# Performance work log

Measured on AMD Instinct MI355X. Metric: run time of the kernel, lower is better.

Reference implementation:

```python
import jax, jax.numpy as jnp
import numpy as np

K_NN = 9  # kernel_size: neighbors per node (includes self, dist 0)


def knn_edges(feat):
    """feat: (B, C, N). Replicates DenseDilatedKnnGraph (dilation=1):
    L2-normalize over channels, dense pairwise sq-distance, top-k nearest."""
    nrm = jnp.sqrt(jnp.sum(feat * feat, axis=1, keepdims=True))
    xn = feat / jnp.maximum(nrm, 1e-12)            # F.normalize(dim=1)
    xt = jnp.swapaxes(xn, 1, 2)                    # (B, N, C)
    sq = jnp.sum(xt * xt, axis=-1)                 # (B, N)
    dist = sq[:, :, None] + sq[:, None, :] - 2.0 * jnp.einsum('bnc,bmc->bnm', xt, xt)
    _, nn_idx = jax.lax.top_k(-dist, K_NN)         # (B, N, k)
    center = jnp.broadcast_to(jnp.arange(nn_idx.shape[1], dtype=nn_idx.dtype)[None, :, None], nn_idx.shape)
    return nn_idx, center                          # (x_j sources, x_i targets)


def reference(x, W0, W1, bias):
    B, C, H, W = x.shape
    N = H * W
    NB = B * N
    feat = x.reshape(B, C, N)
    # KNN graph is built on detached features in the torch source
    x_j, x_i = knn_edges(jax.lax.stop_gradient(feat))
    E = B * N * K_NN
    # faithful to source: torch.linspace(0, B, steps=E, dtype=int64) batch offsets
    count = jnp.linspace(0.0, float(B), E).astype(jnp.int32)
    src = x_j.reshape(-1).astype(jnp.int32) + count * N
    dst = x_i.reshape(-1).astype(jnp.int32) + count * N
    valid = (src < NB) & (dst < NB)                # drop the out-of-range tail edge
    # flat_nodes: (B, C, H, W) -> (B*H*W, C), node id = b*HW + pixel
    nodes = jnp.swapaxes(feat, 1, 2).reshape(NB, C)
    # ChebConv K=2, sym norm, lambda_max=2: Tx0 = x, Tx1 = -(D^-1/2 A D^-1/2) x
    w = valid.astype(nodes.dtype)
    deg = jax.ops.segment_sum(w, src, num_segments=NB)
    dinv = jnp.where(deg > 0, jax.lax.rsqrt(jnp.maximum(deg, 1.0)), 0.0)
    norm = -(dinv[src] * w * dinv[dst])            # scaled-Laplacian edge weights
    msg = norm[:, None] * nodes[src]               # (E, C) gather + weight
    Tx1 = jax.ops.segment_sum(msg, dst, num_segments=NB)
    return nodes @ W0 + Tx1 @ W1 + bias


def setup_inputs() -> dict:
    key = jax.random.key(0)
    k1, k2, k3, k4 = jax.random.split(key, 4)
    B, C, H, W = 8, 48, 64, 64
    Cout = 48
    s = 1.0 / np.sqrt(C)
    return {
        'x': jax.random.normal(k1, (B, C, H, W), dtype=jnp.float32),
        'W0': jax.random.normal(k2, (C, Cout), dtype=jnp.float32) * s,
        'W1': jax.random.normal(k3, (C, Cout), dtype=jnp.float32) * s,
        'bias': jax.random.normal(k4, (Cout,), dtype=jnp.float32) * 0.01,
    }
```

## Files before the change

kernel.cpp:

```cpp
#include <hip/hip_runtime.h>

#define BATCH 8
#define CH    48
#define NPTS  4096
#define NBN   (BATCH*NPTS)
#define KNN   9
#define NCAND 12

typedef unsigned short u16;
typedef unsigned int   u32;
typedef unsigned long long u64;
typedef __bf16 bf16x8 __attribute__((ext_vector_type(8)));
typedef float  f32x4  __attribute__((ext_vector_type(4)));

__device__ __forceinline__ float bf2f(u16 v) { return __uint_as_float(((u32)v) << 16); }
__device__ __forceinline__ u16 f2bf(float f) {
  u32 u = __float_as_uint(f);
  u = (u + 0x7fffu + ((u >> 16) & 1u)) >> 16;
  return (u16)u;
}

__global__ __launch_bounds__(256)
void k_prep(const float* __restrict__ x, float* __restrict__ xraw,
            float* __restrict__ xn, float* __restrict__ csq,
            u16* __restrict__ Abuf, u16* __restrict__ Bbuf,
            int* __restrict__ deg) {
  int node = blockIdx.x * 256 + threadIdx.x;
  deg[node] = 0;
  int b = node >> 12, n = node & (NPTS - 1);
  const float* xb = x + (size_t)b * CH * NPTS;
  float f[CH];
#pragma unroll
  for (int c = 0; c < CH; ++c) f[c] = xb[(size_t)c * NPTS + n];
  float a0 = 0, a1 = 0, a2 = 0, a3 = 0;
#pragma unroll
  for (int k = 0; k < CH; k += 4) {
    a0 += f[k] * f[k]; a1 += f[k+1] * f[k+1];
    a2 += f[k+2] * f[k+2]; a3 += f[k+3] * f[k+3];
  }
  float nrm = fmaxf(sqrtf((a0 + a1) + (a2 + a3)), 1e-12f);
  float xv[CH];
#pragma unroll
  for (int c = 0; c < CH; ++c) xv[c] = f[c] / nrm;
  a0 = a1 = a2 = a3 = 0;
#pragma unroll
  for (int k = 0; k < CH; k += 4) {
    a0 += xv[k] * xv[k]; a1 += xv[k+1] * xv[k+1];
    a2 += xv[k+2] * xv[k+2]; a3 += xv[k+3] * xv[k+3];
  }
  float csqv = (a0 + a1) + (a2 + a3);
  csq[node] = csqv;
  float4* ro = (float4*)(xraw + (size_t)node * CH);
  float4* no = (float4*)(xn   + (size_t)node * CH);
#pragma unroll
  for (int i = 0; i < CH / 4; ++i) {
    ro[i] = make_float4(f[4*i], f[4*i+1], f[4*i+2], f[4*i+3]);
    no[i] = make_float4(xv[4*i], xv[4*i+1], xv[4*i+2], xv[4*i+3]);
  }
  u16 ah[64], al[64];
#pragma unroll
  for (int k = 0; k < CH; ++k) {
    float av = -2.0f * xv[k];
    u16 h = f2bf(av); ah[k] = h; al[k] = f2bf(av - bf2f(h));
  }
  { u16 h = f2bf(csqv); ah[48] = h; al[48] = f2bf(csqv - bf2f(h)); }
#pragma unroll
  for (int k = 49; k < 64; ++k) { ah[k] = 0; al[k] = 0; }
  u16* Bh = Bbuf + (size_t)node * 128;
#pragma unroll
  for (int k = 0; k < CH; ++k) {
    float bv = xv[k];
    u16 h = f2bf(bv); Bh[k] = h; Bh[64 + k] = f2bf(bv - bf2f(h));
  }
  Bh[48] = 0x3F80; Bh[64 + 48] = 0;
#pragma unroll
  for (int k = 49; k < 64; ++k) { Bh[k] = 0; Bh[64 + k] = 0; }
  u16* Ag = Abuf + (size_t)(node >> 4) * 2048 + (size_t)(node & 15) * 8;
#pragma unroll
  for (int v = 0; v < 4; ++v) {
    const u16* src = (v < 2) ? ah : al;
    int koff = (v & 1) * 32;
#pragma unroll
    for (int q = 0; q < 4; ++q) {
      uint4 pk;
      const u16* s = src + koff + q * 8;
      pk.x = (u32)s[0] | ((u32)s[1] << 16);
      pk.y = (u32)s[2] | ((u32)s[3] << 16);
      pk.z = (u32)s[4] | ((u32)s[5] << 16);
      pk.w = (u32)s[6] | ((u32)s[7] << 16);
      *(uint4*)(Ag + v * 512 + q * 128) = pk;
    }
  }
}

#define MED3(d, a, b, c) \
  asm("v_med3_u32 %0, %1, %2, %3" : "=v"(d) : "v"(a), "v"(b), "v"(c))
#define INSERT12(x) do { \
  MED3(s11, s10, s11, x); MED3(s10, s9, s10, x); MED3(s9, s8, s9, x);  \
  MED3(s8,  s7,  s8,  x); MED3(s7,  s6, s7,  x); MED3(s6, s5, s6, x);  \
  MED3(s5,  s4,  s5,  x); MED3(s4,  s3, s4,  x); MED3(s3, s2, s3, x);  \
  MED3(s2,  s1,  s2,  x); MED3(s1,  s0, s1,  x); s0 = min(s0, x);      \
} while (0)

__global__ __launch_bounds__(256, 6)
void k_knn_m(const u16* __restrict__ Abuf, const u16* __restrict__ Bbuf,
             u64* __restrict__ candu) {
  int tid = threadIdx.x;
  int lane = tid & 63;
  int quad = lane >> 4, m16 = lane & 15;
  int panel = blockIdx.x * 4 + (tid >> 6);
  int row = panel * 16 + m16;
  int b4096 = row & ~(NPTS - 1);
  int quarter = blockIdx.y;
  int ct0 = quarter * 64;

  const __bf16* Bb = (const __bf16*)Bbuf + (size_t)row * 128;
  bf16x8 bh0 = *(const bf16x8*)(Bb + quad * 8);
  bf16x8 bh1 = *(const bf16x8*)(Bb + 32 + quad * 8);
  bf16x8 bl0 = *(const bf16x8*)(Bb + 64 + quad * 8);
  bf16x8 bl1 = *(const bf16x8*)(Bb + 96 + quad * 8);

  const __bf16* Ag = (const __bf16*)Abuf + (size_t)(b4096 >> 4) * 2048
                     + (size_t)lane * 8 + (size_t)ct0 * 2048;

  u32 s0=~0u,s1=~0u,s2=~0u,s3=~0u,s4=~0u,s5=~0u,
      s6=~0u,s7=~0u,s8=~0u,s9=~0u,s10=~0u,s11=~0u;

  bf16x8 a0 = *(const bf16x8*)(Ag);
  bf16x8 a1 = *(const bf16x8*)(Ag + 512);
  bf16x8 a2 = *(const bf16x8*)(Ag + 1024);
  bf16x8 a3 = *(const bf16x8*)(Ag + 1536);

  for (int t = 0; t < 64; ++t) {
    const __bf16* apn = Ag + (size_t)((t < 63) ? (t + 1) : 63) * 2048;
    bf16x8 n0 = *(const bf16x8*)(apn);
    bf16x8 n1 = *(const bf16x8*)(apn + 512);
    bf16x8 n2 = *(const bf16x8*)(apn + 1024);
    bf16x8 n3 = *(const bf16x8*)(apn + 1536);

    f32x4 acc = {2.5f, 2.5f, 2.5f, 2.5f};
    acc = __builtin_amdgcn_mfma_f32_16x16x32_bf16(a0, bh0, acc, 0, 0, 0);
    acc = __builtin_amdgcn_mfma_f32_16x16x32_bf16(a1, bh1, acc, 0, 0, 0);
    acc = __builtin_amdgcn_mfma_f32_16x16x32_bf16(a0, bl0, acc, 0, 0, 0);
    acc = __builtin_amdgcn_mfma_f32_16x16x32_bf16(a1, bl1, acc, 0, 0, 0);
    acc = __builtin_amdgcn_mfma_f32_16x16x32_bf16(a2, bh0, acc, 0, 0, 0);
    acc = __builtin_amdgcn_mfma_f32_16x16x32_bf16(a3, bh1, acc, 0, 0, 0);
    int ct = ct0 + t;
#pragma unroll
    for (int r = 0; r < 4; ++r) {
      u32 u = __float_as_uint(acc[r]);
      u32 x = (u & 0xFFFFFC00u) | (u32)((ct << 2) | r);
      INSERT12(x);
    }
    a0 = n0; a1 = n1; a2 = n2; a3 = n3;
  }

  u64* o = candu + (((size_t)row * 4 + quarter) * 4 + quad) * NCAND;
#define EMIT(j, sv) { u32 col = ((sv & 0x3FFu) >> 2) * 16 + quad * 4 + (sv & 3u); \
                      o[j] = ((u64)sv << 12) | (u64)col; }
  EMIT(0, s0)  EMIT(1, s1)  EMIT(2, s2)  EMIT(3, s3)
  EMIT(4, s4)  EMIT(5, s5)  EMIT(6, s6)  EMIT(7, s7)
  EMIT(8, s8)  EMIT(9, s9)  EMIT(10, s10) EMIT(11, s11)
#undef EMIT
}

#define STEP64(si) { u64 _lo = (x < si) ? x : si; u64 _hi = (x < si) ? si : x; \
                     si = _lo; x = _hi; }
__global__ __launch_bounds__(256, 4)
void k_reduce(const u64* __restrict__ candu, u32* __restrict__ cand12) {
  __shared__ u64 ls[64 * 4 * NCAND];
  int tid = threadIdx.x;
  int lr = tid >> 2, q = tid & 3;
  int row = blockIdx.x * 64 + lr;
  const u64* src = candu + (size_t)row * 192 + q * 48;
  u64 t0=~0ull,t1=~0ull,t2=~0ull,t3=~0ull,t4=~0ull,t5=~0ull,
      t6=~0ull,t7=~0ull,t8=~0ull,t9=~0ull,t10=~0ull,t11=~0ull;
  for (int s = 0; s < 48; ++s) {
    u64 x = src[s];
    STEP64(t0) STEP64(t1) STEP64(t2) STEP64(t3) STEP64(t4) STEP64(t5)
    STEP64(t6) STEP64(t7) STEP64(t8) STEP64(t9) STEP64(t10) STEP64(t11)
  }
  u64* lw = ls + (size_t)(lr * 4 + q) * NCAND;
  lw[0]=t0; lw[1]=t1; lw[2]=t2; lw[3]=t3; lw[4]=t4; lw[5]=t5;
  lw[6]=t6; lw[7]=t7; lw[8]=t8; lw[9]=t9; lw[10]=t10; lw[11]=t11;
  __syncthreads();
  if (q == 0) {
    u64 g0=~0ull,g1=~0ull,g2=~0ull,g3=~0ull,g4=~0ull,g5=~0ull,
        g6=~0ull,g7=~0ull,g8=~0ull,g9=~0ull,g10=~0ull,g11=~0ull;
    const u64* lsrc = ls + (size_t)lr * 48;
    for (int s = 0; s < 48; ++s) {
      u64 x = lsrc[s];
      STEP64(g0) STEP64(g1) STEP64(g2) STEP64(g3) STEP64(g4) STEP64(g5)
      STEP64(g6) STEP64(g7) STEP64(g8) STEP64(g9) STEP64(g10) STEP64(g11)
    }
    u32* o = cand12 + (size_t)row * NCAND;
    o[0]=(u32)(g0&0xFFFu); o[1]=(u32)(g1&0xFFFu); o[2]=(u32)(g2&0xFFFu);
    o[3]=(u32)(g3&0xFFFu); o[4]=(u32)(g4&0xFFFu); o[5]=(u32)(g5&0xFFFu);
    o[6]=(u32)(g6&0xFFFu); o[7]=(u32)(g7&0xFFFu); o[8]=(u32)(g8&0xFFFu);
    o[9]=(u32)(g9&0xFFFu); o[10]=(u32)(g10&0xFFFu); o[11]=(u32)(g11&0xFFFu);
  }
}

#define RR 16
__global__ __launch_bounds__(256, 4)
void k_rescore(const float* __restrict__ xn, const float* __restrict__ csq,
               const u32* __restrict__ cand12,
               u16* __restrict__ nn, int* __restrict__ deg) {
  __shared__ float dS[RR * NCAND];
  __shared__ int   iS[RR * NCAND];
  int tid = threadIdx.x;
  int lr = tid >> 4, q = tid & 15;
  int bi = blockIdx.x;
  int row = (bi & 7) * NPTS + (bi >> 3) * RR + lr;
  int b4096 = row & ~(NPTS - 1);
  const float* xnb = xn + (size_t)b4096 * CH;
  if (q < NCAND) {
    float rf[CH];
    const float4* p = (const float4*)(xn + (size_t)row * CH);
#pragma unroll
    for (int i = 0; i < CH / 4; ++i) {
      float4 v = p[i];
      rf[4*i] = v.x; rf[4*i+1] = v.y; rf[4*i+2] = v.z; rf[4*i+3] = v.w;
    }
    float sqn = csq[row];
    int c = (int)(cand12[(size_t)row * NCAND + q] & (NPTS - 1));
    const float4* cp = (const float4*)(xnb + (size_t)c * CH);
    float a0 = 0, a1 = 0, a2 = 0, a3 = 0;
#pragma unroll
    for (int i = 0; i < CH / 4; ++i) {
      float4 v = cp[i];
      a0 += rf[4*i]   * v.x; a1 += rf[4*i+1] * v.y;
      a2 += rf[4*i+2] * v.z; a3 += rf[4*i+3] * v.w;
    }
    float dist = (sqn + csq[b4096 + c]) - 2.0f * ((a0 + a1) + (a2 + a3));
    dS[lr * NCAND + q] = dist;
    iS[lr * NCAND + q] = c;
  }
  __syncthreads();
  if (q == 0) {
    float gd[KNN]; int gi[KNN];
#pragma unroll
    for (int j = 0; j < KNN; ++j) { gd[j] = 3.4e38f; gi[j] = 0x7fffffff; }
    for (int s = 0; s < NCAND; ++s) {
      float dc = dS[lr * NCAND + s]; int ic = iS[lr * NCAND + s];
      if (dc < gd[KNN - 1] || (dc == gd[KNN - 1] && ic < gi[KNN - 1])) {
        gd[KNN - 1] = dc; gi[KNN - 1] = ic;
#pragma unroll
        for (int k2 = KNN - 1; k2 > 0; --k2) {
          bool sw = (gd[k2] < gd[k2 - 1]) ||
                    (gd[k2] == gd[k2 - 1] && gi[k2] < gi[k2 - 1]);
          if (sw) {
            float td = gd[k2]; gd[k2] = gd[k2 - 1]; gd[k2 - 1] = td;
            int ti = gi[k2]; gi[k2] = gi[k2 - 1]; gi[k2 - 1] = ti;
          }
        }
      }
    }
    u16* o = nn + (size_t)row * KNN;
    int jmax = (row == NBN - 1) ? (KNN - 1) : KNN;
#pragma unroll
    for (int j = 0; j < KNN; ++j) o[j] = (u16)(gi[j] & (NPTS - 1));
    for (int j = 0; j < jmax; ++j)
      atomicAdd(&deg[b4096 + (gi[j] & (NPTS - 1))], 1);
  }
}

#define ONB 64
#define LPAD 52
__global__ __launch_bounds__(256)
void k_out_f(const float* __restrict__ xraw, const u16* __restrict__ nn,
             const int* __restrict__ deg,
             const float* __restrict__ W0, const float* __restrict__ W1,
             const float* __restrict__ bias, float* __restrict__ out) {
  __shared__ float w0[CH * CH], w1[CH * CH], bs[CH];
  __shared__ __align__(16) float fS[ONB * LPAD];
  __shared__ __align__(16) float txS[ONB * LPAD];
  __shared__ float dinvS[ONB];
  int tid = threadIdx.x;
  int bi = blockIdx.x;
  int n0 = (bi & 7) * NPTS + (bi >> 3) * ONB;
  int b12 = n0 & ~(NPTS - 1);
  for (int i = tid; i < CH * CH; i += 256) { w0[i] = W0[i]; w1[i] = W1[i]; }
  if (tid < CH) bs[tid] = bias[tid];
  for (int i = tid; i < ONB * 12; i += 256) {
    int ln = i / 12, f4 = i % 12;
    *(float4*)(fS + ln * LPAD + f4 * 4) =
        *(const float4*)(xraw + (size_t)(n0 + ln) * CH + f4 * 4);
  }
  if (tid < ONB) {
    int dg = deg[n0 + tid];
    dinvS[tid] = (dg > 0) ? (1.0f / sqrtf((float)dg)) : 0.0f;
  }
  __syncthreads();

  int ln = tid >> 2, p = tid & 3;
  int node = n0 + ln;
  float dn = dinvS[ln];
  const u16* nrow = nn + (size_t)node * KNN;
  bool full = (node != NBN - 1);
  float tx[12];
#pragma unroll
  for (int i = 0; i < 12; ++i) tx[i] = 0.f;
#pragma unroll
  for (int j = 0; j < KNN; ++j) {
    if (j < KNN - 1 || full) {
      int s = nrow[j] & (NPTS - 1);
      int dgs = deg[b12 + s];
      float ds = (dgs > 0) ? (1.0f / sqrtf((float)dgs)) : 0.0f;
      float w = -(ds * dn);
      const float4* pr = (const float4*)(xraw + (size_t)(b12 + s) * CH + p * 12);
#pragma unroll
      for (int q3 = 0; q3 < 3; ++q3) {
        float4 v = pr[q3];
        tx[q3*4]   += w * v.x; tx[q3*4+1] += w * v.y;
        tx[q3*4+2] += w * v.z; tx[q3*4+3] += w * v.w;
      }
    }
  }
#pragma unroll
  for (int q3 = 0; q3 < 3; ++q3)
    *(float4*)(txS + ln * LPAD + p * 12 + q3 * 4) =
        make_float4(tx[q3*4], tx[q3*4+1], tx[q3*4+2], tx[q3*4+3]);
  __syncthreads();

  float acc[12];
#pragma unroll
  for (int i = 0; i < 12; ++i) acc[i] = bs[p * 12 + i];
  const float* fr = fS + ln * LPAD;
  const float* tr = txS + ln * LPAD;
#pragma unroll
  for (int c = 0; c < CH; ++c) {
    float fc = fr[c];
    const float* wr = w0 + c * CH + p * 12;
#pragma unroll
    for (int i = 0; i < 12; ++i) acc[i] += fc * wr[i];
  }
#pragma unroll
  for (int c = 0; c < CH; ++c) {
    float tc = tr[c];
    const float* wr = w1 + c * CH + p * 12;
#pragma unroll
    for (int i = 0; i < 12; ++i) acc[i] += tc * wr[i];
  }
  float* op = out + (size_t)node * CH + p * 12;
#pragma unroll
  for (int q3 = 0; q3 < 3; ++q3)
    *(float4*)(op + q3 * 4) =
        make_float4(acc[q3*4], acc[q3*4+1], acc[q3*4+2], acc[q3*4+3]);
}

__global__ __launch_bounds__(256)
void k_zero(int* __restrict__ deg) { deg[blockIdx.x * 256 + threadIdx.x] = 0; }

__global__ __launch_bounds__(256)
void k_hist(const u16* __restrict__ nn, int* __restrict__ deg) {
  int node = blockIdx.x * 256 + threadIdx.x;
  int b12 = node & ~(NPTS - 1);
  int jmax = (node == NBN - 1) ? (KNN - 1) : KNN;
  for (int j = 0; j < jmax; ++j)
    atomicAdd(&deg[b12 + (nn[(size_t)node * KNN + j] & (NPTS - 1))], 1);
}

__global__ __launch_bounds__(256)
void k_dinv(const int* __restrict__ deg, float* __restrict__ dinv) {
  int i = blockIdx.x * 256 + threadIdx.x;
  int dg = deg[i];
  dinv[i] = (dg > 0) ? (1.0f / sqrtf((float)dg)) : 0.0f;
}

#define NQ    4
#define QCOLS (NPTS/NQ)
#define TCOLS 32
#define NTILES (QCOLS/TCOLS)
#define RPB   64

__global__ __launch_bounds__(256)
void k_knn_nb(const float* __restrict__ x, u16* __restrict__ nn) {
  __shared__ __align__(16) float tile[NQ * TCOLS * CH];
  __shared__ float nrmS[NQ * TCOLS];
  __shared__ float csq[NQ * TCOLS];
  int tid = threadIdx.x;
  int r0 = blockIdx.x * RPB;
  int b  = r0 >> 12;
  int q  = tid >> 6;
  int lr = tid & 63;
  int n  = (r0 + lr) & (NPTS - 1);
  const float* xb = x + (size_t)b * CH * NPTS;
  float rf[CH];
#pragma unroll
  for (int c = 0; c < CH; ++c) rf[c] = xb[(size_t)c * NPTS + n];
  float sqn;
  {
    float a0 = 0, a1 = 0, a2 = 0, a3 = 0;
#pragma unroll
    for (int k = 0; k < CH; k += 4) {
      a0 += rf[k] * rf[k]; a1 += rf[k+1] * rf[k+1];
      a2 += rf[k+2] * rf[k+2]; a3 += rf[k+3] * rf[k+3];
    }
    float nrm = fmaxf(sqrtf((a0 + a1) + (a2 + a3)), 1e-12f);
#pragma unroll
    for (int c = 0; c < CH; ++c) rf[c] = rf[c] / nrm;
    a0 = a1 = a2 = a3 = 0;
#pragma unroll
    for (int k = 0; k < CH; k += 4) {
      a0 += rf[k] * rf[k]; a1 += rf[k+1] * rf[k+1];
      a2 += rf[k+2] * rf[k+2]; a3 += rf[k+3] * rf[k+3];
    }
    sqn = (a0 + a1) + (a2 + a3);
  }
  float d[KNN]; int id[KNN];
#pragma unroll
  for (int j = 0; j < KNN; ++j) { d[j] = 3.4e38f; id[j] = 0x7fffffff; }
  for (int t = 0; t < NTILES; ++t) {
    __syncthreads();
#pragma unroll
    for (int qq = 0; qq < NQ; ++qq) {
      int colbase = qq * QCOLS + t * TCOLS;
      float* dst = tile + qq * TCOLS * CH;
#pragma unroll
      for (int it = 0; it < 6; ++it) {
        int i = it * 256 + tid;
        int c = i >> 5, p = i & 31;
        dst[p * CH + c] = xb[(size_t)c * NPTS + colbase + p];
      }
    }
    __syncthreads();
    if (tid < NQ * TCOLS) {
      const float* cp = tile + tid * CH;
      float a0 = 0, a1 = 0, a2 = 0, a3 = 0;
#pragma unroll
      for (int k = 0; k < CH; k += 4) {
        float4 v = *(const float4*)(cp + k);
        a0 += v.x * v.x; a1 += v.y * v.y; a2 += v.z * v.z; a3 += v.w * v.w;
      }
      nrmS[tid] = fmaxf(sqrtf((a0 + a1) + (a2 + a3)), 1e-12f);
    }
    __syncthreads();
    for (int i = tid; i < NQ * TCOLS * CH; i += 256)
      tile[i] = tile[i] / nrmS[i / CH];
    __syncthreads();
    if (tid < NQ * TCOLS) {
      const float* cp = tile + tid * CH;
      float a0 = 0, a1 = 0, a2 = 0, a3 = 0;
#pragma unroll
      for (int k = 0; k < CH; k += 4) {
        float4 v = *(const float4*)(cp + k);
        a0 += v.x * v.x; a1 += v.y * v.y; a2 += v.z * v.z; a3 += v.w * v.w;
      }
      csq[tid] = (a0 + a1) + (a2 + a3);
    }
    __syncthreads();
    int cbase = q * QCOLS + t * TCOLS;
    const float* tq = tile + q * TCOLS * CH;
    for (int cc = 0; cc < TCOLS; ++cc) {
      const float* cp = tq + cc * CH;
      float a0 = 0, a1 = 0, a2 = 0, a3 = 0;
#pragma unroll
      for (int k = 0; k < CH; k += 4) {
        float4 v = *(const float4*)(cp + k);
        a0 += rf[k] * v.x; a1 += rf[k+1] * v.y;
        a2 += rf[k+2] * v.z; a3 += rf[k+3] * v.w;
      }
      float dist = (sqn + csq[q * TCOLS + cc]) - 2.0f * ((a0 + a1) + (a2 + a3));
      if (dist < d[KNN - 1]) {
        d[KNN - 1] = dist; id[KNN - 1] = cbase + cc;
#pragma unroll
        for (int k2 = KNN - 1; k2 > 0; --k2) {
          if (d[k2] < d[k2 - 1]) {
            float td = d[k2]; d[k2] = d[k2 - 1]; d[k2 - 1] = td;
            int ti = id[k2]; id[k2] = id[k2 - 1]; id[k2 - 1] = ti;
          }
        }
      }
    }
  }
  __syncthreads();
  float* md = tile;
  int*   mi = (int*)(tile + 256 * KNN);
#pragma unroll
  for (int j = 0; j < KNN; ++j) { md[tid * KNN + j] = d[j]; mi[tid * KNN + j] = id[j]; }
  __syncthreads();
  if (tid < RPB) {
    float fd[KNN]; int fi[KNN];
#pragma unroll
    for (int j = 0; j < KNN; ++j) { fd[j] = 3.4e38f; fi[j] = 0x7fffffff; }
    for (int qq = 0; qq < NQ; ++qq) {
      int s = qq * RPB + tid;
      for (int j = 0; j < KNN; ++j) {
        float dc = md[s * KNN + j]; int ic = mi[s * KNN + j];
        if (dc < fd[KNN - 1]) {
          fd[KNN - 1] = dc; fi[KNN - 1] = ic;
#pragma unroll
          for (int k2 = KNN - 1; k2 > 0; --k2) {
            if (fd[k2] < fd[k2 - 1]) {
              float td = fd[k2]; fd[k2] = fd[k2 - 1]; fd[k2 - 1] = td;
              int ti = fi[k2]; fi[k2] = fi[k2 - 1]; fi[k2 - 1] = ti;
            }
          }
        }
      }
    }
    u16* o = nn + (size_t)(r0 + tid) * KNN;
#pragma unroll
    for (int j = 0; j < KNN; ++j) o[j] = (u16)(fi[j] & (NPTS - 1));
  }
}

__global__ __launch_bounds__(256)
void k_out_nb(const float* __restrict__ x, const u16* __restrict__ nn,
              const float* __restrict__ dinv,
              const float* __restrict__ W0, const float* __restrict__ W1,
              const float* __restrict__ bias, float* __restrict__ out) {
  __shared__ float w0[CH * CH], w1[CH * CH], bs[CH];
  for (int i = threadIdx.x; i < CH * CH; i += 256) { w0[i] = W0[i]; w1[i] = W1[i]; }
  if (threadIdx.x < CH) bs[threadIdx.x] = bias[threadIdx.x];
  __syncthreads();
  int node = blockIdx.x * 256 + threadIdx.x;
  int b = node >> 12, n = node & (NPTS - 1);
  const float* xb = x + (size_t)b * CH * NPTS;
  float f[CH], acc[CH], tx[CH];
#pragma unroll
  for (int c = 0; c < CH; ++c) f[c] = xb[(size_t)c * NPTS + n];
#pragma unroll
  for (int o = 0; o < CH; ++o) acc[o] = bs[o];
#pragma unroll
  for (int c = 0; c < CH; ++c) {
    float fc = f[c];
    const float* wr = w0 + c * CH;
#pragma unroll
    for (int o = 0; o < CH; ++o) acc[o] += fc * wr[o];
  }
#pragma unroll
  for (int c = 0; c < CH; ++c) tx[c] = 0.f;
  float dn = dinv[node];
  int jmax = (node == NBN - 1) ? (KNN - 1) : KNN;
  for (int j = 0; j < jmax; ++j) {
    int s = nn[(size_t)node * KNN + j] & (NPTS - 1);
    float w = -(dinv[(b << 12) + s] * dn);
#pragma unroll
    for (int c = 0; c < CH; ++c) tx[c] += w * xb[(size_t)c * NPTS + s];
  }
#pragma unroll
  for (int c = 0; c < CH; ++c) {
    float tc = tx[c];
    const float* wr = w1 + c * CH;
#pragma unroll
    for (int o = 0; o < CH; ++o) acc[o] += tc * wr[o];
  }
  float4* op = (float4*)(out + (size_t)node * CH);
#pragma unroll
  for (int i = 0; i < CH / 4; ++i)
    op[i] = make_float4(acc[4*i], acc[4*i+1], acc[4*i+2], acc[4*i+3]);
}

extern "C" void kernel_launch(void* const* d_in, const int* in_sizes, int n_in,
                              void* d_out, int out_size, void* d_ws, size_t ws_size,
                              hipStream_t stream) {
  const float* x    = (const float*)d_in[0];
  const float* W0   = (const float*)d_in[1];
  const float* W1   = (const float*)d_in[2];
  const float* bias = (const float*)d_in[3];
  float* out = (float*)d_out;
  char* w = (char*)d_ws;

  const size_t SZ_XN   = (size_t)NBN * CH * 4;
  const size_t SZ_XRAW = (size_t)NBN * CH * 4;
  const size_t SZ_CSQ  = (size_t)NBN * 4;
  const size_t SZ_NN   = (size_t)NBN * KNN * 2;
  const size_t SZ_DEG  = (size_t)NBN * 4;
  const size_t SZ_AB   = (size_t)NBN * 128 * 2;
  const size_t SZ_CU   = (size_t)NBN * 16 * NCAND * 8;
  const size_t SZ_C12  = (size_t)NBN * NCAND * 4;
  const size_t needF = SZ_XN + SZ_XRAW + SZ_CSQ + SZ_NN + SZ_DEG
                     + 2 * SZ_AB + SZ_CU + SZ_C12;

  if (ws_size >= needF) {
    size_t off = 0;
    float* xn   = (float*)(w + off); off += SZ_XN;
    float* xraw = (float*)(w + off); off += SZ_XRAW;
    float* csq  = (float*)(w + off); off += SZ_CSQ;
    u16*   nn   = (u16*)  (w + off); off += SZ_NN;
    int*   deg  = (int*)  (w + off); off += SZ_DEG;
    u16*   Abuf = (u16*)  (w + off); off += SZ_AB;
    u16*   Bbuf = (u16*)  (w + off); off += SZ_AB;
    u64*   candu= (u64*)  (w + off); off += SZ_CU;
    u32*   cand12=(u32*)  (w + off);
    k_prep    <<<NBN / 256, 256, 0, stream>>>(x, xraw, xn, csq, Abuf, Bbuf, deg);
    k_knn_m   <<<dim3(NBN / 64, 4), 256, 0, stream>>>(Abuf, Bbuf, candu);
    k_reduce  <<<NBN / 64, 256, 0, stream>>>(candu, cand12);
    k_rescore <<<NBN / RR, 256, 0, stream>>>(xn, csq, cand12, nn, deg);
    k_out_f   <<<NBN / ONB, 256, 0, stream>>>(xraw, nn, deg, W0, W1, bias, out);
  } else {
    u16*   nn   = (u16*)w;
    int*   deg  = (int*)(w + SZ_NN);
    float* dinv = (float*)(w + SZ_NN + SZ_DEG);
    k_knn_nb <<<NBN / RPB, 256, 0, stream>>>(x, nn);
    k_zero   <<<NBN / 256, 256, 0, stream>>>(deg);
    k_hist   <<<NBN / 256, 256, 0, stream>>>(nn, deg);
    k_dinv   <<<NBN / 256, 256, 0, stream>>>(deg, dinv);
    k_out_nb <<<NBN / 256, 256, 0, stream>>>(x, nn, dinv, W0, W1, bias, out);
  }
}
```

Baseline: 240.1 us.

## Pack candidates into 32-bit keys and unroll KNN tile loop by two

The KNN scoring kernel now packs the full 12-bit column index into the low bits of each 32-bit distance key, so candidates are stored as u32 instead of u64. The reduce kernel then uses v_med3_u32 insertion on 32-bit keys rather than 64-bit compare-swap chains, halving candidate memory traffic and LDS use. The tile loop is unrolled by two with double-buffered A loads to overlap loads with MFMA and the insertion work, and the occupancy hint drops from 6 to 4 waves. Dropping two more mantissa bits from the distance key coarsens the ordering, which may change tie resolution among near-equal candidates.

```diff
diff --git a/kernel.cpp b/kernel.cpp
--- a/kernel.cpp
+++ b/kernel.cpp
@@ -19,6 +19,15 @@
   u = (u + 0x7fffu + ((u >> 16) & 1u)) >> 16;
   return (u16)u;
 }
+
+#define MED3U(d, a, b, c) \
+  asm("v_med3_u32 %0, %1, %2, %3" : "=v"(d) : "v"(a), "v"(b), "v"(c))
+#define INS12(p0,p1,p2,p3,p4,p5,p6,p7,p8,p9,p10,p11,x) do { \
+  MED3U(p11,p10,p11,x); MED3U(p10,p9,p10,x); MED3U(p9,p8,p9,x);  \
+  MED3U(p8, p7, p8, x); MED3U(p7, p6,p7, x); MED3U(p6,p5,p6,x);  \
+  MED3U(p5, p4, p5, x); MED3U(p4, p3,p4, x); MED3U(p3,p2,p3,x);  \
+  MED3U(p2, p1, p2, x); MED3U(p1, p0,p1, x); p0 = min(p0, x);    \
+} while (0)
 
 __global__ __launch_bounds__(256)
 void k_prep(const float* __restrict__ x, float* __restrict__ xraw,
@@ -93,18 +102,9 @@
   }
 }
 
-#define MED3(d, a, b, c) \
-  asm("v_med3_u32 %0, %1, %2, %3" : "=v"(d) : "v"(a), "v"(b), "v"(c))
-#define INSERT12(x) do { \
-  MED3(s11, s10, s11, x); MED3(s10, s9, s10, x); MED3(s9, s8, s9, x);  \
-  MED3(s8,  s7,  s8,  x); MED3(s7,  s6, s7,  x); MED3(s6, s5, s6, x);  \
-  MED3(s5,  s4,  s5,  x); MED3(s4,  s3, s4,  x); MED3(s3, s2, s3, x);  \
-  MED3(s2,  s1,  s2,  x); MED3(s1,  s0, s1,  x); s0 = min(s0, x);      \
-} while (0)
-
-__global__ __launch_bounds__(256, 6)
+__global__ __launch_bounds__(256, 4)
 void k_knn_m(const u16* __restrict__ Abuf, const u16* __restrict__ Bbuf,
-             u64* __restrict__ candu) {
+             u32* __restrict__ candu) {
   int tid = threadIdx.x;
   int lane = tid & 63;
   int quad = lane >> 4, m16 = lane & 15;
@@ -126,78 +126,82 @@
   u32 s0=~0u,s1=~0u,s2=~0u,s3=~0u,s4=~0u,s5=~0u,
       s6=~0u,s7=~0u,s8=~0u,s9=~0u,s10=~0u,s11=~0u;
 
+#define TILE_BODY(A0,A1,A2,A3,CT) do {                                      \
+    f32x4 acc = {2.5f, 2.5f, 2.5f, 2.5f};                                   \
+    acc = __builtin_amdgcn_mfma_f32_16x16x32_bf16(A0, bh0, acc, 0, 0, 0);   \
+    acc = __builtin_amdgcn_mfma_f32_16x16x32_bf16(A1, bh1, acc, 0, 0, 0);   \
+    acc = __builtin_amdgcn_mfma_f32_16x16x32_bf16(A0, bl0, acc, 0, 0, 0);   \
+    acc = __builtin_amdgcn_mfma_f32_16x16x32_bf16(A1, bl1, acc, 0, 0, 0);   \
+    acc = __builtin_amdgcn_mfma_f32_16x16x32_bf16(A2, bh0, acc, 0, 0, 0);   \
+    acc = __builtin_amdgcn_mfma_f32_16x16x32_bf16(A3, bh1, acc, 0, 0, 0);   \
+    u32 colb = ((u32)(CT) << 4) | ((u32)quad << 2);                         \
+    _Pragma("unroll")                                                       \
+    for (int r = 0; r < 4; ++r) {                                           \
+      u32 u = __float_as_uint(acc[r]);                                      \
+      u32 xx = (u & 0xFFFFF000u) | (colb | (u32)r);                         \
+      INS12(s0,s1,s2,s3,s4,s5,s6,s7,s8,s9,s10,s11, xx);                     \
+    }                                                                       \
+  } while (0)
+
   bf16x8 a0 = *(const bf16x8*)(Ag);
   bf16x8 a1 = *(const bf16x8*)(Ag + 512);
   bf16x8 a2 = *(const bf16x8*)(Ag + 1024);
   bf16x8 a3 = *(const bf16x8*)(Ag + 1536);
 
-  for (int t = 0; t < 64; ++t) {
-    const __bf16* apn = Ag + (size_t)((t < 63) ? (t + 1) : 63) * 2048;
-    bf16x8 n0 = *(const bf16x8*)(apn);
-    bf16x8 n1 = *(const bf16x8*)(apn + 512);
-    bf16x8 n2 = *(const bf16x8*)(apn + 1024);
-    bf16x8 n3 = *(const bf16x8*)(apn + 1536);
-
-    f32x4 acc = {2.5f, 2.5f, 2.5f, 2.5f};
-    acc = __builtin_amdgcn_mfma_f32_16x16x32_bf16(a0, bh0, acc, 0, 0, 0);
-    acc = __builtin_amdgcn_mfma_f32_16x16x32_bf16(a1, bh1, acc, 0, 0, 0);
-    acc = __builtin_amdgcn_mfma_f32_16x16x32_bf16(a0, bl0, acc, 0, 0, 0);
-    acc = __builtin_amdgcn_mfma_f32_16x16x32_bf16(a1, bl1, acc, 0, 0, 0);
-    acc = __builtin_amdgcn_mfma_f32_16x16x32_bf16(a2, bh0, acc, 0, 0, 0);
-    acc = __builtin_amdgcn_mfma_f32_16x16x32_bf16(a3, bh1, acc, 0, 0, 0);
-    int ct = ct0 + t;
-#pragma unroll
-    for (int r = 0; r < 4; ++r) {
-      u32 u = __float_as_uint(acc[r]);
-      u32 x = (u & 0xFFFFFC00u) | (u32)((ct << 2) | r);
-      INSERT12(x);
-    }
-    a0 = n0; a1 = n1; a2 = n2; a3 = n3;
-  }
-
-  u64* o = candu + (((size_t)row * 4 + quarter) * 4 + quad) * NCAND;
-#define EMIT(j, sv) { u32 col = ((sv & 0x3FFu) >> 2) * 16 + quad * 4 + (sv & 3u); \
-                      o[j] = ((u64)sv << 12) | (u64)col; }
-  EMIT(0, s0)  EMIT(1, s1)  EMIT(2, s2)  EMIT(3, s3)
-  EMIT(4, s4)  EMIT(5, s5)  EMIT(6, s6)  EMIT(7, s7)
-  EMIT(8, s8)  EMIT(9, s9)  EMIT(10, s10) EMIT(11, s11)
-#undef EMIT
-}
-
-#define STEP64(si) { u64 _lo = (x < si) ? x : si; u64 _hi = (x < si) ? si : x; \
-                     si = _lo; x = _hi; }
+  for (int t = 0; t < 64; t += 2) {
+    const __bf16* apc = Ag + (size_t)(t + 1) * 2048;
+    bf16x8 c0 = *(const bf16x8*)(apc);
+    bf16x8 c1 = *(const bf16x8*)(apc + 512);
+    bf16x8 c2 = *(const bf16x8*)(apc + 1024);
+    bf16x8 c3 = *(const bf16x8*)(apc + 1536);
+
+    TILE_BODY(a0, a1, a2, a3, ct0 + t);
+
+    const __bf16* apn = Ag + (size_t)((t + 2 < 64) ? (t + 2) : 63) * 2048;
+    a0 = *(const bf16x8*)(apn);
+    a1 = *(const bf16x8*)(apn + 512);
+    a2 = *(const bf16x8*)(apn + 1024);
+    a3 = *(const bf16x8*)(apn + 1536);
+
+    TILE_BODY(c0, c1, c2, c3, ct0 + t + 1);
+  }
+#undef TILE_BODY
+
+  u32* o = candu + (((size_t)row * 4 + quarter) * 4 + quad) * NCAND;
+  o[0]=s0; o[1]=s1; o[2]=s2; o[3]=s3; o[4]=s4; o[5]=s5;
+  o[6]=s6; o[7]=s7; o[8]=s8; o[9]=s9; o[10]=s10; o[11]=s11;
+}
+
 __global__ __launch_bounds__(256, 4)
-void k_reduce(const u64* __restrict__ candu, u32* __restrict__ cand12) {
-  __shared__ u64 ls[64 * 4 * NCAND];
+void k_reduce(const u32* __restrict__ candu, u32* __restrict__ cand12) {
+  __shared__ u32 ls[64 * 4 * NCAND];
   int tid = threadIdx.x;
   int lr = tid >> 2, q = tid & 3;
   int row = blockIdx.x * 64 + lr;
-  const u64* src = candu + (size_t)row * 192 + q * 48;
-  u64 t0=~0ull,t1=~0ull,t2=~0ull,t3=~0ull,t4=~0ull,t5=~0ull,
-      t6=~0ull,t7=~0ull,t8=~0ull,t9=~0ull,t10=~0ull,t11=~0ull;
+  const u32* src = candu + (size_t)row * 192 + q * 48;
+  u32 t0=~0u,t1=~0u,t2=~0u,t3=~0u,t4=~0u,t5=~0u,
+      t6=~0u,t7=~0u,t8=~0u,t9=~0u,t10=~0u,t11=~0u;
   for (int s = 0; s < 48; ++s) {
-    u64 x = src[s];
-    STEP64(t0) STEP64(t1) STEP64(t2) STEP64(t3) STEP64(t4) STEP64(t5)
-    STEP64(t6) STEP64(t7) STEP64(t8) STEP64(t9) STEP64(t10) STEP64(t11)
-  }
-  u64* lw = ls + (size_t)(lr * 4 + q) * NCAND;
+    u32 x = src[s];
+    INS12(t0,t1,t2,t3,t4,t5,t6,t7,t8,t9,t10,t11, x);
+  }
+  u32* lw = ls + (size_t)(lr * 4 + q) * NCAND;
   lw[0]=t0; lw[1]=t1; lw[2]=t2; lw[3]=t3; lw[4]=t4; lw[5]=t5;
   lw[6]=t6; lw[7]=t7; lw[8]=t8; lw[9]=t9; lw[10]=t10; lw[11]=t11;
   __syncthreads();
   if (q == 0) {
-    u64 g0=~0ull,g1=~0ull,g2=~0ull,g3=~0ull,g4=~0ull,g5=~0ull,
-        g6=~0ull,g7=~0ull,g8=~0ull,g9=~0ull,g10=~0ull,g11=~0ull;
-    const u64* lsrc = ls + (size_t)lr * 48;
+    u32 g0=~0u,g1=~0u,g2=~0u,g3=~0u,g4=~0u,g5=~0u,
+        g6=~0u,g7=~0u,g8=~0u,g9=~0u,g10=~0u,g11=~0u;
+    const u32* lsrc = ls + (size_t)lr * 48;
     for (int s = 0; s < 48; ++s) {
-      u64 x = lsrc[s];
-      STEP64(g0) STEP64(g1) STEP64(g2) STEP64(g3) STEP64(g4) STEP64(g5)
-      STEP64(g6) STEP64(g7) STEP64(g8) STEP64(g9) STEP64(g10) STEP64(g11)
+      u32 x = lsrc[s];
+      INS12(g0,g1,g2,g3,g4,g5,g6,g7,g8,g9,g10,g11, x);
     }
     u32* o = cand12 + (size_t)row * NCAND;
-    o[0]=(u32)(g0&0xFFFu); o[1]=(u32)(g1&0xFFFu); o[2]=(u32)(g2&0xFFFu);
-    o[3]=(u32)(g3&0xFFFu); o[4]=(u32)(g4&0xFFFu); o[5]=(u32)(g5&0xFFFu);
-    o[6]=(u32)(g6&0xFFFu); o[7]=(u32)(g7&0xFFFu); o[8]=(u32)(g8&0xFFFu);
-    o[9]=(u32)(g9&0xFFFu); o[10]=(u32)(g10&0xFFFu); o[11]=(u32)(g11&0xFFFu);
+    o[0]=(g0&0xFFFu); o[1]=(g1&0xFFFu); o[2]=(g2&0xFFFu);
+    o[3]=(g3&0xFFFu); o[4]=(g4&0xFFFu); o[5]=(g5&0xFFFu);
+    o[6]=(g6&0xFFFu); o[7]=(g7&0xFFFu); o[8]=(g8&0xFFFu);
+    o[9]=(g9&0xFFFu); o[10]=(g10&0xFFFu); o[11]=(g11&0xFFFu);
   }
 }
 
@@ -569,7 +573,7 @@
   const size_t SZ_NN   = (size_t)NBN * KNN * 2;
   const size_t SZ_DEG  = (size_t)NBN * 4;
   const size_t SZ_AB   = (size_t)NBN * 128 * 2;
-  const size_t SZ_CU   = (size_t)NBN * 16 * NCAND * 8;
+  const size_t SZ_CU   = (size_t)NBN * 16 * NCAND * 4;
   const size_t SZ_C12  = (size_t)NBN * NCAND * 4;
   const size_t needF = SZ_XN + SZ_XRAW + SZ_CSQ + SZ_NN + SZ_DEG
                      + 2 * SZ_AB + SZ_CU + SZ_C12;
@@ -583,7 +587,7 @@
     int*   deg  = (int*)  (w + off); off += SZ_DEG;
     u16*   Abuf = (u16*)  (w + off); off += SZ_AB;
     u16*   Bbuf = (u16*)  (w + off); off += SZ_AB;
-    u64*   candu= (u64*)  (w + off); off += SZ_CU;
+    u32*   candu= (u32*)  (w + off); off += SZ_CU;
     u32*   cand12=(u32*)  (w + off);
     k_prep    <<<NBN / 256, 256, 0, stream>>>(x, xraw, xn, csq, Abuf, Bbuf, deg);
     k_knn_m   <<<dim3(NBN / 64, 4), 256, 0, stream>>>(Abuf, Bbuf, candu);
```

Result: faster. 225.5 us (-6.1%).
